# Kernel optimization log

Measured on AMD Instinct MI355X. Metric: run time of the kernel, lower is better.

Reference implementation:

```python
import jax, jax.numpy as jnp
import numpy as np

B, N, DH = 8, 2048, 512
EPS = 1e-5


def _layer_norm(x, g, b):
    m = x.mean(-1, keepdims=True)
    v = ((x - m) ** 2).mean(-1, keepdims=True)
    return (x - m) * jax.lax.rsqrt(v + EPS) * g + b


def setup_inputs() -> dict:
    key = jax.random.key(0)
    ks = jax.random.split(key, 20)
    s = 1.0 / np.sqrt(DH)
    sf = 1.0 / np.sqrt(2 * DH)
    return {
        "H": jax.random.normal(ks[0], (B, N, DH), jnp.float32),
        "adj": jax.random.uniform(ks[1], (B, N, N), jnp.float32),
        "hop_emb": jax.random.normal(ks[2], (N, DH), jnp.float32),
        "Wq": jax.random.normal(ks[3], (DH, DH), jnp.float32) * s,
        "bq": jnp.zeros((DH,), jnp.float32),
        "Wk": jax.random.normal(ks[4], (DH, DH), jnp.float32) * s,
        "bk": jnp.zeros((DH,), jnp.float32),
        "Wv": jax.random.normal(ks[5], (DH, DH), jnp.float32) * s,
        "bv": jnp.zeros((DH,), jnp.float32),
        "W1": jax.random.normal(ks[6], (DH, 2 * DH), jnp.float32) * s,
        "b1": jnp.zeros((2 * DH,), jnp.float32),
        "W2": jax.random.normal(ks[7], (2 * DH, DH), jnp.float32) * sf,
        "b2": jnp.zeros((DH,), jnp.float32),
        "g1": jnp.ones((DH,), jnp.float32),
        "be1": jnp.zeros((DH,), jnp.float32),
        "g2": jnp.ones((DH,), jnp.float32),
        "be2": jnp.zeros((DH,), jnp.float32),
    }


def reference(H, adj, hop_emb, Wq, bq, Wk, bk, Wv, bv, W1, b1, W2, b2, g1, be1, g2, be2):
    Q = H @ Wq + bq                                     # [B,N,DH]
    K = H @ Wk + bk
    V = H @ Wv + bv
    scores = jnp.einsum("bid,bjd->bij", Q, K) / np.sqrt(DH).astype(np.float32)
    # (adj[...,None] * hop_emb).mean(-1) == adj * hop_emb.mean(-1)[j]
    hop_effect = adj * hop_emb.mean(-1)[None, None, :]  # [B,N,N]
    attn = jax.nn.softmax(scores * hop_effect, axis=-1)
    attn_out = jnp.einsum("bij,bjd->bid", attn, V)
    x = _layer_norm(attn_out + H, g1, be1)
    ffn = jax.nn.relu(x @ W1 + b1) @ W2 + b2
    return _layer_norm(ffn + x, g2, be2)
```

## Files before the change

kernel.cpp:

```cpp
#include <hip/hip_runtime.h>

typedef unsigned short u16;
typedef __bf16 bf16x8 __attribute__((ext_vector_type(8)));
typedef float f32x4 __attribute__((ext_vector_type(4)));

#define SEQN 2048
#define DHID 512

static __device__ __forceinline__ float bf2f(u16 u) {
    union { unsigned int i; float f; } c; c.i = ((unsigned int)u) << 16; return c.f;
}
static __device__ __forceinline__ u16 f2bf(float f) {
    union { float f; unsigned int i; } c; c.f = f;
    unsigned int x = c.i;
    return (u16)((x + 0x7fffu + ((x >> 16) & 1u)) >> 16);
}

static __device__ __forceinline__ void gld_lds16(const u16* g, u16* l) {
    __builtin_amdgcn_global_load_lds(
        (__attribute__((address_space(1))) void*)(g),
        (__attribute__((address_space(3))) void*)(l), 16, 0, 0);
}

__global__ __launch_bounds__(256) void cvt_kernel(const float* __restrict__ src,
                                                  u16* __restrict__ dst, int n) {
    int i = (blockIdx.x * 256 + threadIdx.x) * 8;
    if (i >= n) return;
    float4 a = *(const float4*)(src + i);
    float4 b = *(const float4*)(src + i + 4);
    union { uint4 u; u16 s[8]; } o;
    o.s[0] = f2bf(a.x); o.s[1] = f2bf(a.y); o.s[2] = f2bf(a.z); o.s[3] = f2bf(a.w);
    o.s[4] = f2bf(b.x); o.s[5] = f2bf(b.y); o.s[6] = f2bf(b.z); o.s[7] = f2bf(b.w);
    *(uint4*)(dst + i) = o.u;
}

__global__ __launch_bounds__(256) void cvt_t_kernel(const float* __restrict__ src,
                                                    u16* __restrict__ dst, int K, int N) {
    int idx = blockIdx.x * 256 + threadIdx.x;
    if (idx >= K * N) return;
    int n = idx / K, k = idx - n * K;
    dst[idx] = f2bf(src[(size_t)k * N + n]);
}

__global__ void hmean_kernel(const float* __restrict__ hop, float* __restrict__ hm) {
    int j = blockIdx.x, t = threadIdx.x;
    const float* p = hop + (size_t)j * DHID + t * 8;
    float4 a = *(const float4*)p;
    float4 b = *(const float4*)(p + 4);
    float s = a.x + a.y + a.z + a.w + b.x + b.y + b.z + b.w;
#pragma unroll
    for (int m = 1; m < 64; m <<= 1) s += __shfl_xor(s, m);
    if (t == 0) hm[j] = s * (1.0f / (float)DHID);
}

enum { EPI_BIAS = 0, EPI_RELU = 1, EPI_PLAIN = 3, EPI_BIAS_T = 4, EPI_QKV = 5 };

template <int EPI>
__global__ __launch_bounds__(256) void gemm_bt(
    const u16* __restrict__ A, const u16* __restrict__ Bt, u16* __restrict__ C,
    const float* __restrict__ bias,
    int K, int lda, int ldb, int ldc,
    u16* __restrict__ Qo, u16* __restrict__ Ko, u16* __restrict__ Vto,
    const float* __restrict__ bq_, const float* __restrict__ bk_,
    const float* __restrict__ bv_)
{
    __shared__ u16 As[128 * 32];
    __shared__ u16 Bs[128 * 32];

    const int tid = threadIdx.x;
    const u16* Ab = A;
    const u16* Bb = Bt;

    const int bm0 = blockIdx.y * 128, bn0 = blockIdx.x * 128;
    const int wid = tid >> 6, lane = tid & 63, quad = lane >> 4, l16 = lane & 15;
    const int wm = (wid >> 1) * 64, wn = (wid & 1) * 64;
    const int srow = lane >> 2;
    const int skof = (lane & 3) * 8;

    f32x4 acc[4][4];
#pragma unroll
    for (int i = 0; i < 4; ++i)
#pragma unroll
        for (int j = 0; j < 4; ++j) acc[i][j] = (f32x4){0.f, 0.f, 0.f, 0.f};

    for (int k0 = 0; k0 < K; k0 += 32) {
#pragma unroll
        for (int it = 0; it < 2; ++it) {
            int c = wid * 2 + it;
            gld_lds16(Ab + (size_t)(bm0 + c * 16 + srow) * lda + k0 + skof,
                      &As[c * 512]);
        }
#pragma unroll
        for (int it = 0; it < 2; ++it) {
            int c = wid * 2 + it;
            gld_lds16(Bb + (size_t)(bn0 + c * 16 + srow) * ldb + k0 + skof,
                      &Bs[c * 512]);
        }
        __syncthreads();

        bf16x8 af[4], bfr[4];
#pragma unroll
        for (int i = 0; i < 4; ++i)
            af[i] = *(const bf16x8*)&As[(wm + i * 16 + l16) * 32 + quad * 8];
#pragma unroll
        for (int j = 0; j < 4; ++j)
            bfr[j] = *(const bf16x8*)&Bs[(wn + j * 16 + l16) * 32 + quad * 8];
#pragma unroll
        for (int i = 0; i < 4; ++i)
#pragma unroll
            for (int j = 0; j < 4; ++j)
                acc[i][j] = __builtin_amdgcn_mfma_f32_16x16x32_bf16(af[i], bfr[j], acc[i][j], 0, 0, 0);
        __syncthreads();
    }

#pragma unroll
    for (int i = 0; i < 4; ++i) {
#pragma unroll
        for (int j = 0; j < 4; ++j) {
            const int gn = bn0 + wn + j * 16 + l16;
            const int gm0 = bm0 + wm + i * 16 + quad * 4;
            if constexpr (EPI == EPI_BIAS || EPI == EPI_RELU) {
                const float b = bias[gn];
#pragma unroll
                for (int r = 0; r < 4; ++r) {
                    float v = acc[i][j][r] + b;
                    if constexpr (EPI == EPI_RELU) v = fmaxf(v, 0.f);
                    C[(size_t)(gm0 + r) * ldc + gn] = f2bf(v);
                }
            } else if constexpr (EPI == EPI_BIAS_T) {
                const float b = bias[gn];
                const int bb = gm0 >> 11, n = gm0 & 2047;
                ushort4 o;
                o.x = f2bf(acc[i][j][0] + b);
                o.y = f2bf(acc[i][j][1] + b);
                o.z = f2bf(acc[i][j][2] + b);
                o.w = f2bf(acc[i][j][3] + b);
                *(ushort4*)&C[((size_t)bb * 512 + gn) * 2048 + n] = o;
            } else if constexpr (EPI == EPI_QKV) {
                const int sel = gn >> 9;
                const int n = gn & 511;
                if (sel == 0) {
                    const float b = bq_[n];
#pragma unroll
                    for (int r = 0; r < 4; ++r)
                        Qo[(size_t)(gm0 + r) * DHID + n] = f2bf(acc[i][j][r] + b);
                } else if (sel == 1) {
                    const float b = bk_[n];
#pragma unroll
                    for (int r = 0; r < 4; ++r)
                        Ko[(size_t)(gm0 + r) * DHID + n] = f2bf(acc[i][j][r] + b);
                } else {
                    const float b = bv_[n];
                    const int bb = gm0 >> 11, nn2 = gm0 & 2047;
                    ushort4 o;
                    o.x = f2bf(acc[i][j][0] + b);
                    o.y = f2bf(acc[i][j][1] + b);
                    o.z = f2bf(acc[i][j][2] + b);
                    o.w = f2bf(acc[i][j][3] + b);
                    *(ushort4*)&Vto[((size_t)bb * 512 + n) * 2048 + nn2] = o;
                }
            } else {
#pragma unroll
                for (int r = 0; r < 4; ++r)
                    C[(size_t)(gm0 + r) * ldc + gn] = f2bf(acc[i][j][r]);
            }
        }
    }
}

__global__ __launch_bounds__(256, 2) void attn_kernel(
    const u16* __restrict__ Q, const u16* __restrict__ K, const u16* __restrict__ Vt,
    const float* __restrict__ adj, const float* __restrict__ hm,
    u16* __restrict__ AO)
{
    extern __shared__ u16 lds[];
    u16* Ks = lds;
    u16* Vs = lds + 16384;
    u16* Pb = lds + 32768;

    const int tid = threadIdx.x, wid = tid >> 6, lane = tid & 63;
    const int quad = lane >> 4, l16 = lane & 15;
    const int b = blockIdx.x;
    const int q0 = blockIdx.y * 32 + (wid >> 1) * 16;
    const int ch = wid & 1;
    const int D0 = ch * 256;
    const int srow = lane >> 2, sko = (lane & 3) * 8;

    const u16* Qg = Q + (size_t)b * SEQN * DHID;
    const u16* Kg = K + (size_t)b * SEQN * DHID;
    const u16* Vg = Vt + (size_t)b * DHID * SEQN;
    const float* adjg = adj + (size_t)b * SEQN * SEQN;
    u16* AOg = AO + (size_t)b * SEQN * DHID;
    const float* arow = adjg + (size_t)(q0 + quad * 4) * SEQN;
    u16* Pg = Pb + (wid >> 1) * 640;

    const float scale = 0.044194173824159216f;

    bf16x8 qf[16];
#pragma unroll
    for (int ds = 0; ds < 16; ++ds)
        qf[ds] = *(const bf16x8*)(Qg + (size_t)(q0 + l16) * DHID + ds * 32 + quad * 8);

    f32x4 oacc[16];
#pragma unroll
    for (int dt = 0; dt < 16; ++dt) oacc[dt] = (f32x4){0.f, 0.f, 0.f, 0.f};
    float lsum[4] = {0.f, 0.f, 0.f, 0.f};

#pragma unroll
    for (int i = 0; i < 8; ++i) {
        int id = wid * 8 + i, ds = id >> 1, c = id & 1;
        gld_lds16(Kg + (size_t)(c * 16 + srow) * DHID + ds * 32 + sko,
                  &Ks[ds * 1024 + c * 512]);
    }

    for (int kt = 0; kt < 64; ++kt) {
        const int kv0 = kt * 32;

        __syncthreads();

#pragma unroll
        for (int i = 0; i < 8; ++i) {
            int id = wid * 8 + i;
            gld_lds16(Vg + (size_t)(id * 16 + srow) * SEQN + kv0 + sko,
                      &Vs[id * 512]);
        }

        float hv = hm[kv0 + ch * 16 + l16] * scale;
        float av[4];
#pragma unroll
        for (int r = 0; r < 4; ++r)
            av[r] = arow[(size_t)r * SEQN + kv0 + ch * 16 + l16];

        f32x4 sa = {0.f,0.f,0.f,0.f}, sb = {0.f,0.f,0.f,0.f};
#pragma unroll
        for (int ds = 0; ds < 16; ds += 2) {
            bf16x8 k0 = *(const bf16x8*)&Ks[ds * 1024 + ch * 512 + l16 * 32 + quad * 8];
            sa = __builtin_amdgcn_mfma_f32_16x16x32_bf16(qf[ds], k0, sa, 0, 0, 0);
            bf16x8 k1 = *(const bf16x8*)&Ks[(ds + 1) * 1024 + ch * 512 + l16 * 32 + quad * 8];
            sb = __builtin_amdgcn_mfma_f32_16x16x32_bf16(qf[ds + 1], k1, sb, 0, 0, 0);
        }
        f32x4 s = sa + sb;

        __syncthreads();

        if (kt < 63) {
#pragma unroll
            for (int i = 0; i < 8; ++i) {
                int id = wid * 8 + i, ds = id >> 1, c = id & 1;
                gld_lds16(Kg + (size_t)(kv0 + 32 + c * 16 + srow) * DHID + ds * 32 + sko,
                          &Ks[ds * 1024 + c * 512]);
            }
        }
        __builtin_amdgcn_sched_barrier(0);

#pragma unroll
        for (int r = 0; r < 4; ++r) {
            float p = __expf(s[r] * av[r] * hv);
            lsum[r] += p;
            Pg[(quad * 4 + r) * 40 + ch * 16 + l16] = f2bf(p);
        }

        asm volatile("s_waitcnt lgkmcnt(0)" ::: "memory");
        __builtin_amdgcn_s_barrier();
        __builtin_amdgcn_sched_barrier(0);

        bf16x8 pf = *(const bf16x8*)&Pg[l16 * 40 + quad * 8];

#pragma unroll
        for (int dt = 0; dt < 16; ++dt) {
            bf16x8 vf = *(const bf16x8*)&Vs[(D0 + dt * 16 + l16) * 32 + quad * 8];
            oacc[dt] = __builtin_amdgcn_mfma_f32_16x16x32_bf16(pf, vf, oacc[dt], 0, 0, 0);
        }
    }

#pragma unroll
    for (int r = 0; r < 4; ++r) {
#pragma unroll
        for (int m = 1; m < 16; m <<= 1) lsum[r] += __shfl_xor(lsum[r], m);
    }
    __syncthreads();
    float* SUMS = (float*)Pb;
    if (l16 == 0) {
#pragma unroll
        for (int r = 0; r < 4; ++r) SUMS[wid * 16 + quad * 4 + r] = lsum[r];
    }
    __syncthreads();
#pragma unroll
    for (int r = 0; r < 4; ++r)
        lsum[r] = 1.f / (lsum[r] + SUMS[(wid ^ 1) * 16 + quad * 4 + r]);

#pragma unroll
    for (int dt = 0; dt < 16; ++dt) {
#pragma unroll
        for (int r = 0; r < 4; ++r) {
            AOg[(size_t)(q0 + quad * 4 + r) * DHID + D0 + dt * 16 + l16] =
                f2bf(oacc[dt][r] * lsum[r]);
        }
    }
}

__global__ __launch_bounds__(256) void ln_hf32_kernel(
    const u16* __restrict__ a, const float* __restrict__ Hf,
    const float* __restrict__ g, const float* __restrict__ be,
    u16* __restrict__ out)
{
    size_t row = blockIdx.x;
    int t = threadIdx.x, wid = t >> 6, lane = t & 63;
    unsigned int va = *(const unsigned int*)(a + row * (size_t)DHID + t * 2);
    float2 h = *(const float2*)(Hf + row * (size_t)DHID + t * 2);
    float x0 = bf2f((u16)(va & 0xffff)) + h.x;
    float x1 = bf2f((u16)(va >> 16)) + h.y;
    float s = x0 + x1, sq = x0 * x0 + x1 * x1;
#pragma unroll
    for (int m = 1; m < 64; m <<= 1) { s += __shfl_xor(s, m); sq += __shfl_xor(sq, m); }
    __shared__ float rs[4], rq[4];
    if (lane == 0) { rs[wid] = s; rq[wid] = sq; }
    __syncthreads();
    s = rs[0] + rs[1] + rs[2] + rs[3];
    sq = rq[0] + rq[1] + rq[2] + rq[3];
    float mean = s * (1.f / (float)DHID);
    float var = sq * (1.f / (float)DHID) - mean * mean;
    float rstd = rsqrtf(var + 1e-5f);
    float2 vg = *(const float2*)(g + t * 2);
    float2 vbe = *(const float2*)(be + t * 2);
    float y0 = (x0 - mean) * rstd * vg.x + vbe.x;
    float y1 = (x1 - mean) * rstd * vg.y + vbe.y;
    unsigned int o = (unsigned int)f2bf(y0) | ((unsigned int)f2bf(y1) << 16);
    *(unsigned int*)(out + row * (size_t)DHID + t * 2) = o;
}

__global__ __launch_bounds__(256) void ln_kernel_f32out(
    const u16* __restrict__ a, const u16* __restrict__ bp,
    const float* __restrict__ g, const float* __restrict__ be,
    float* __restrict__ out)
{
    size_t row = blockIdx.x;
    int t = threadIdx.x, wid = t >> 6, lane = t & 63;
    unsigned int va = *(const unsigned int*)(a + row * (size_t)DHID + t * 2);
    unsigned int vb = *(const unsigned int*)(bp + row * (size_t)DHID + t * 2);
    float x0 = bf2f((u16)(va & 0xffff)) + bf2f((u16)(vb & 0xffff));
    float x1 = bf2f((u16)(va >> 16)) + bf2f((u16)(vb >> 16));
    float s = x0 + x1, sq = x0 * x0 + x1 * x1;
#pragma unroll
    for (int m = 1; m < 64; m <<= 1) { s += __shfl_xor(s, m); sq += __shfl_xor(sq, m); }
    __shared__ float rs[4], rq[4];
    if (lane == 0) { rs[wid] = s; rq[wid] = sq; }
    __syncthreads();
    s = rs[0] + rs[1] + rs[2] + rs[3];
    sq = rq[0] + rq[1] + rq[2] + rq[3];
    float mean = s * (1.f / (float)DHID);
    float var = sq * (1.f / (float)DHID) - mean * mean;
    float rstd = rsqrtf(var + 1e-5f);
    float2 vg = *(const float2*)(g + t * 2);
    float2 vbe = *(const float2*)(be + t * 2);
    float y0 = (x0 - mean) * rstd * vg.x + vbe.x;
    float y1 = (x1 - mean) * rstd * vg.y + vbe.y;
    *(float2*)(out + row * (size_t)DHID + t * 2) = make_float2(y0, y1);
}

extern "C" void kernel_launch(void* const* d_in, const int* in_sizes, int n_in,
                              void* d_out, int out_size, void* d_ws, size_t ws_size,
                              hipStream_t stream) {
    const float* H   = (const float*)d_in[0];
    const float* adj = (const float*)d_in[1];
    const float* hop = (const float*)d_in[2];
    const float* Wq  = (const float*)d_in[3];
    const float* bq  = (const float*)d_in[4];
    const float* Wk  = (const float*)d_in[5];
    const float* bk  = (const float*)d_in[6];
    const float* Wv  = (const float*)d_in[7];
    const float* bv  = (const float*)d_in[8];
    const float* W1  = (const float*)d_in[9];
    const float* b1  = (const float*)d_in[10];
    const float* W2  = (const float*)d_in[11];
    const float* b2  = (const float*)d_in[12];
    const float* g1  = (const float*)d_in[13];
    const float* be1 = (const float*)d_in[14];
    const float* g2  = (const float*)d_in[15];
    const float* be2 = (const float*)d_in[16];

    const size_t MiB = 1ull << 20;
    char* w = (char*)d_ws;
    float* hm   = (float*)w;
    u16* Hb    = (u16*)(w + 1 * MiB);
    u16* Wqkvt = (u16*)(w + 17 * MiB);
    u16* W1t   = (u16*)(w + 18 * MiB + 512 * 1024);
    u16* W2t   = (u16*)(w + 19 * MiB + 512 * 1024);
    u16* Q     = (u16*)(w + 21 * MiB);
    u16* Kb    = (u16*)(w + 37 * MiB);
    u16* Vt    = (u16*)(w + 53 * MiB);
    u16* AO    = (u16*)(w + 69 * MiB);
    u16* HID   = (u16*)(w + 85 * MiB);
    u16* X   = Kb;
    u16* F2  = Vt;

    const int BN = 8, N = SEQN, D = DHID;

    cvt_kernel<<<(BN * N * D) / (8 * 256), 256, 0, stream>>>(H, Hb, BN * N * D);
    cvt_t_kernel<<<(D * D + 255) / 256, 256, 0, stream>>>(Wq, Wqkvt, D, D);
    cvt_t_kernel<<<(D * D + 255) / 256, 256, 0, stream>>>(Wk, Wqkvt + D * D, D, D);
    cvt_t_kernel<<<(D * D + 255) / 256, 256, 0, stream>>>(Wv, Wqkvt + 2 * D * D, D, D);
    cvt_t_kernel<<<(D * 2 * D + 255) / 256, 256, 0, stream>>>(W1, W1t, D, 2 * D);
    cvt_t_kernel<<<(2 * D * D + 255) / 256, 256, 0, stream>>>(W2, W2t, 2 * D, D);

    hmean_kernel<<<N, 64, 0, stream>>>(hop, hm);

    gemm_bt<EPI_QKV><<<dim3(12, 128, 1), 256, 0, stream>>>(
        Hb, Wqkvt, nullptr, nullptr, D, D, D, 0, Q, Kb, Vt, bq, bk, bv);

    attn_kernel<<<dim3(8, 64), 256, 68096, stream>>>(Q, Kb, Vt, adj, hm, AO);

    ln_hf32_kernel<<<BN * N, 256, 0, stream>>>(AO, H, g1, be1, X);

    gemm_bt<EPI_RELU><<<dim3(8, 128, 1), 256, 0, stream>>>(
        X, W1t, HID, b1, D, D, D, 2 * D, nullptr, nullptr, nullptr, nullptr, nullptr, nullptr);

    gemm_bt<EPI_BIAS><<<dim3(4, 128, 1), 256, 0, stream>>>(
        HID, W2t, F2, b2, 2 * D, 2 * D, 2 * D, D, nullptr, nullptr, nullptr, nullptr, nullptr, nullptr);

    ln_kernel_f32out<<<BN * N, 256, 0, stream>>>(F2, X, g2, be2, (float*)d_out);
}
```

Measured before the change: 556.2 us.

## Use 32x32 MFMA for PV with shared P tile and XOR-swizzled K/V LDS

The P·V product in the attention kernel now uses 32x32x16 MFMA instructions. All four waves read the full 32-row P tile and each wave owns a 128-column slice of the output dimension, replacing the earlier 16x16 MFMA per row-group and half-D split. K and V tiles in LDS are stored with an XOR swizzle on the 16-byte chunk index to reduce bank conflicts on fragment reads. The epilogue and row-sum exchange are remapped to the 32x32 accumulator layout. The cost is more complex index math, and every wave must wait on the full shared P tile.

```diff
diff --git a/kernel.cpp b/kernel.cpp
--- a/kernel.cpp
+++ b/kernel.cpp
@@ -3,6 +3,7 @@
 typedef unsigned short u16;
 typedef __bf16 bf16x8 __attribute__((ext_vector_type(8)));
 typedef float f32x4 __attribute__((ext_vector_type(4)));
+typedef float f32x16 __attribute__((ext_vector_type(16)));
 
 #define SEQN 2048
 #define DHID 512
@@ -176,15 +177,17 @@
     extern __shared__ u16 lds[];
     u16* Ks = lds;
     u16* Vs = lds + 16384;
-    u16* Pb = lds + 32768;
+    u16* Pm = lds + 32768;
 
     const int tid = threadIdx.x, wid = tid >> 6, lane = tid & 63;
     const int quad = lane >> 4, l16 = lane & 15;
     const int b = blockIdx.x;
-    const int q0 = blockIdx.y * 32 + (wid >> 1) * 16;
+    const int qblk = blockIdx.y * 32;
+    const int g = wid >> 1;
+    const int q0 = qblk + g * 16;
     const int ch = wid & 1;
-    const int D0 = ch * 256;
-    const int srow = lane >> 2, sko = (lane & 3) * 8;
+    const int srow = lane >> 2;
+    const int skosw = (((lane & 3) ^ (srow & 3)) * 8);
 
     const u16* Qg = Q + (size_t)b * SEQN * DHID;
     const u16* Kg = K + (size_t)b * SEQN * DHID;
@@ -192,7 +195,6 @@
     const float* adjg = adj + (size_t)b * SEQN * SEQN;
     u16* AOg = AO + (size_t)b * SEQN * DHID;
     const float* arow = adjg + (size_t)(q0 + quad * 4) * SEQN;
-    u16* Pg = Pb + (wid >> 1) * 640;
 
     const float scale = 0.044194173824159216f;
 
@@ -201,15 +203,17 @@
     for (int ds = 0; ds < 16; ++ds)
         qf[ds] = *(const bf16x8*)(Qg + (size_t)(q0 + l16) * DHID + ds * 32 + quad * 8);
 
-    f32x4 oacc[16];
-#pragma unroll
-    for (int dt = 0; dt < 16; ++dt) oacc[dt] = (f32x4){0.f, 0.f, 0.f, 0.f};
+    f32x16 oacc[4];
+#pragma unroll
+    for (int t = 0; t < 4; ++t)
+#pragma unroll
+        for (int r = 0; r < 16; ++r) oacc[t][r] = 0.f;
     float lsum[4] = {0.f, 0.f, 0.f, 0.f};
 
 #pragma unroll
     for (int i = 0; i < 8; ++i) {
         int id = wid * 8 + i, ds = id >> 1, c = id & 1;
-        gld_lds16(Kg + (size_t)(c * 16 + srow) * DHID + ds * 32 + sko,
+        gld_lds16(Kg + (size_t)(c * 16 + srow) * DHID + ds * 32 + skosw,
                   &Ks[ds * 1024 + c * 512]);
     }
 
@@ -221,7 +225,7 @@
 #pragma unroll
         for (int i = 0; i < 8; ++i) {
             int id = wid * 8 + i;
-            gld_lds16(Vg + (size_t)(id * 16 + srow) * SEQN + kv0 + sko,
+            gld_lds16(Vg + (size_t)(id * 16 + srow) * SEQN + kv0 + skosw,
                       &Vs[id * 512]);
         }
 
@@ -234,9 +238,11 @@
         f32x4 sa = {0.f,0.f,0.f,0.f}, sb = {0.f,0.f,0.f,0.f};
 #pragma unroll
         for (int ds = 0; ds < 16; ds += 2) {
-            bf16x8 k0 = *(const bf16x8*)&Ks[ds * 1024 + ch * 512 + l16 * 32 + quad * 8];
+            bf16x8 k0 = *(const bf16x8*)&Ks[ds * 1024 + ch * 512 + l16 * 32
+                                            + ((quad ^ (l16 & 3)) * 8)];
             sa = __builtin_amdgcn_mfma_f32_16x16x32_bf16(qf[ds], k0, sa, 0, 0, 0);
-            bf16x8 k1 = *(const bf16x8*)&Ks[(ds + 1) * 1024 + ch * 512 + l16 * 32 + quad * 8];
+            bf16x8 k1 = *(const bf16x8*)&Ks[(ds + 1) * 1024 + ch * 512 + l16 * 32
+                                            + ((quad ^ (l16 & 3)) * 8)];
             sb = __builtin_amdgcn_mfma_f32_16x16x32_bf16(qf[ds + 1], k1, sb, 0, 0, 0);
         }
         f32x4 s = sa + sb;
@@ -247,7 +253,7 @@
 #pragma unroll
             for (int i = 0; i < 8; ++i) {
                 int id = wid * 8 + i, ds = id >> 1, c = id & 1;
-                gld_lds16(Kg + (size_t)(kv0 + 32 + c * 16 + srow) * DHID + ds * 32 + sko,
+                gld_lds16(Kg + (size_t)(kv0 + 32 + c * 16 + srow) * DHID + ds * 32 + skosw,
                           &Ks[ds * 1024 + c * 512]);
             }
         }
@@ -257,19 +263,22 @@
         for (int r = 0; r < 4; ++r) {
             float p = __expf(s[r] * av[r] * hv);
             lsum[r] += p;
-            Pg[(quad * 4 + r) * 40 + ch * 16 + l16] = f2bf(p);
+            Pm[(g * 16 + quad * 4 + r) * 40 + ch * 16 + l16] = f2bf(p);
         }
 
         asm volatile("s_waitcnt lgkmcnt(0)" ::: "memory");
         __builtin_amdgcn_s_barrier();
         __builtin_amdgcn_sched_barrier(0);
 
-        bf16x8 pf = *(const bf16x8*)&Pg[l16 * 40 + quad * 8];
-
-#pragma unroll
-        for (int dt = 0; dt < 16; ++dt) {
-            bf16x8 vf = *(const bf16x8*)&Vs[(D0 + dt * 16 + l16) * 32 + quad * 8];
-            oacc[dt] = __builtin_amdgcn_mfma_f32_16x16x32_bf16(pf, vf, oacc[dt], 0, 0, 0);
+        bf16x8 pa0 = *(const bf16x8*)&Pm[(lane & 31) * 40 + (lane >> 5) * 8];
+        bf16x8 pa1 = *(const bf16x8*)&Pm[(lane & 31) * 40 + 16 + (lane >> 5) * 8];
+#pragma unroll
+        for (int t = 0; t < 4; ++t) {
+            const int d = wid * 128 + t * 32 + (lane & 31);
+            bf16x8 v0 = *(const bf16x8*)&Vs[d * 32 + (((lane >> 5) ^ (d & 3)) * 8)];
+            oacc[t] = __builtin_amdgcn_mfma_f32_32x32x16_bf16(pa0, v0, oacc[t], 0, 0, 0);
+            bf16x8 v1 = *(const bf16x8*)&Vs[d * 32 + (((2 + (lane >> 5)) ^ (d & 3)) * 8)];
+            oacc[t] = __builtin_amdgcn_mfma_f32_32x32x16_bf16(pa1, v1, oacc[t], 0, 0, 0);
         }
     }
 
@@ -279,22 +288,26 @@
         for (int m = 1; m < 16; m <<= 1) lsum[r] += __shfl_xor(lsum[r], m);
     }
     __syncthreads();
-    float* SUMS = (float*)Pb;
+    float* SUMS = (float*)Pm;
     if (l16 == 0) {
 #pragma unroll
-        for (int r = 0; r < 4; ++r) SUMS[wid * 16 + quad * 4 + r] = lsum[r];
+        for (int r = 0; r < 4; ++r)
+            SUMS[ch * 32 + g * 16 + quad * 4 + r] = lsum[r];
     }
     __syncthreads();
-#pragma unroll
-    for (int r = 0; r < 4; ++r)
-        lsum[r] = 1.f / (lsum[r] + SUMS[(wid ^ 1) * 16 + quad * 4 + r]);
-
-#pragma unroll
-    for (int dt = 0; dt < 16; ++dt) {
-#pragma unroll
-        for (int r = 0; r < 4; ++r) {
-            AOg[(size_t)(q0 + quad * 4 + r) * DHID + D0 + dt * 16 + l16] =
-                f2bf(oacc[dt][r] * lsum[r]);
+    float inv16[16];
+#pragma unroll
+    for (int rg = 0; rg < 16; ++rg) {
+        int row = (rg & 3) + 8 * (rg >> 2) + 4 * (lane >> 5);
+        inv16[rg] = 1.f / (SUMS[row] + SUMS[32 + row]);
+    }
+#pragma unroll
+    for (int t = 0; t < 4; ++t) {
+#pragma unroll
+        for (int rg = 0; rg < 16; ++rg) {
+            int row = (rg & 3) + 8 * (rg >> 2) + 4 * (lane >> 5);
+            AOg[(size_t)(qblk + row) * DHID + wid * 128 + t * 32 + (lane & 31)] =
+                f2bf(oacc[t][rg] * inv16[rg]);
         }
     }
 }
```

Measured after the change: 559.6 us. Within noise of the previous version (+0.6%).

## Double-buffer LDS tiles in gemm_bt to prefetch the next K slice

Applied to the files above, without the earlier changes.

Splits the A and B shared-memory tiles into two buffers. Each iteration issues the asynchronous global-to-LDS loads for the next K slice before running the MFMAs on the current one, so the fetch overlaps with compute. This also lets the loop drop to one barrier per iteration instead of two. The cost is twice the LDS per block, which may lower occupancy.

```diff
diff --git a/kernel.cpp b/kernel.cpp
--- a/kernel.cpp
+++ b/kernel.cpp
@@ -64,8 +64,8 @@
     const float* __restrict__ bq_, const float* __restrict__ bk_,
     const float* __restrict__ bv_)
 {
-    __shared__ u16 As[128 * 32];
-    __shared__ u16 Bs[128 * 32];
+    __shared__ u16 As[2][128 * 32];
+    __shared__ u16 Bs[2][128 * 32];
 
     const int tid = threadIdx.x;
     const u16* Ab = A;
@@ -83,34 +83,49 @@
 #pragma unroll
         for (int j = 0; j < 4; ++j) acc[i][j] = (f32x4){0.f, 0.f, 0.f, 0.f};
 
-    for (int k0 = 0; k0 < K; k0 += 32) {
-#pragma unroll
-        for (int it = 0; it < 2; ++it) {
-            int c = wid * 2 + it;
-            gld_lds16(Ab + (size_t)(bm0 + c * 16 + srow) * lda + k0 + skof,
-                      &As[c * 512]);
-        }
-#pragma unroll
-        for (int it = 0; it < 2; ++it) {
-            int c = wid * 2 + it;
-            gld_lds16(Bb + (size_t)(bn0 + c * 16 + srow) * ldb + k0 + skof,
-                      &Bs[c * 512]);
-        }
+#pragma unroll
+    for (int it = 0; it < 2; ++it) {
+        int c = wid * 2 + it;
+        gld_lds16(Ab + (size_t)(bm0 + c * 16 + srow) * lda + skof, &As[0][c * 512]);
+    }
+#pragma unroll
+    for (int it = 0; it < 2; ++it) {
+        int c = wid * 2 + it;
+        gld_lds16(Bb + (size_t)(bn0 + c * 16 + srow) * ldb + skof, &Bs[0][c * 512]);
+    }
+
+    int cur = 0;
+    for (int k0 = 0; k0 < K; k0 += 32, cur ^= 1) {
         __syncthreads();
 
+        if (k0 + 32 < K) {
+#pragma unroll
+            for (int it = 0; it < 2; ++it) {
+                int c = wid * 2 + it;
+                gld_lds16(Ab + (size_t)(bm0 + c * 16 + srow) * lda + k0 + 32 + skof,
+                          &As[cur ^ 1][c * 512]);
+            }
+#pragma unroll
+            for (int it = 0; it < 2; ++it) {
+                int c = wid * 2 + it;
+                gld_lds16(Bb + (size_t)(bn0 + c * 16 + srow) * ldb + k0 + 32 + skof,
+                          &Bs[cur ^ 1][c * 512]);
+            }
+        }
+        __builtin_amdgcn_sched_barrier(0);
+
         bf16x8 af[4], bfr[4];
 #pragma unroll
         for (int i = 0; i < 4; ++i)
-            af[i] = *(const bf16x8*)&As[(wm + i * 16 + l16) * 32 + quad * 8];
+            af[i] = *(const bf16x8*)&As[cur][(wm + i * 16 + l16) * 32 + quad * 8];
 #pragma unroll
         for (int j = 0; j < 4; ++j)
-            bfr[j] = *(const bf16x8*)&Bs[(wn + j * 16 + l16) * 32 + quad * 8];
+            bfr[j] = *(const bf16x8*)&Bs[cur][(wn + j * 16 + l16) * 32 + quad * 8];
 #pragma unroll
         for (int i = 0; i < 4; ++i)
 #pragma unroll
             for (int j = 0; j < 4; ++j)
                 acc[i][j] = __builtin_amdgcn_mfma_f32_16x16x32_bf16(af[i], bfr[j], acc[i][j], 0, 0, 0);
-        __syncthreads();
     }
 
 #pragma unroll
```

After: 549.8 us. No clear change (-1.2%).
